# Performance work log

Measured on AMD Instinct MI355X. Metric: run time of the kernel, lower is better.

The kernel has to match this reference:

```python
import jax, jax.numpy as jnp
import numpy as np

N = 50000      # nodes
E = 100000     # edges
F_NODE = 128
F_EDGE = 16
H = 64         # hidden_dim
OUT = 32
STEPS = 3
G = 64         # num_graphs (static; batch.max()+1 in torch)


def setup_inputs() -> dict:
    key = jax.random.key(0)
    ks = jax.random.split(key, 20)

    def lin(k, fin, fout):
        s = 1.0 / np.sqrt(fin)
        return jax.random.uniform(k, (fin, fout), jnp.float32, -s, s)

    def bias(k, fin, fout):
        s = 1.0 / np.sqrt(fin)
        return jax.random.uniform(k, (fout,), jnp.float32, -s, s)

    inp = {
        'x': jax.random.normal(ks[0], (N, F_NODE), jnp.float32),
        'edge_index': jax.random.randint(ks[1], (2, E), 0, N),
        'edge_attr': jax.random.normal(ks[2], (E, F_EDGE), jnp.float32),
        'batch': jnp.sort(jax.random.randint(ks[3], (N,), 0, G)),
        # node encoder
        'W_enc': lin(ks[4], F_NODE, H), 'b_enc': bias(ks[5], F_NODE, H),
        # edge_nn: Linear(F_EDGE,H) -> ReLU -> Linear(H, H*H)
        'W_e1': lin(ks[6], F_EDGE, H), 'b_e1': bias(ks[7], F_EDGE, H),
        'W_e2': lin(ks[8], H, H * H), 'b_e2': bias(ks[9], H, H * H),
        # GRUCell (torch layout: [3H, H])
        'W_ih': jax.random.uniform(ks[10], (3 * H, H), jnp.float32, -1/np.sqrt(H), 1/np.sqrt(H)),
        'W_hh': jax.random.uniform(ks[11], (3 * H, H), jnp.float32, -1/np.sqrt(H), 1/np.sqrt(H)),
        'b_ih': jax.random.uniform(ks[12], (3 * H,), jnp.float32, -1/np.sqrt(H), 1/np.sqrt(H)),
        'b_hh': jax.random.uniform(ks[13], (3 * H,), jnp.float32, -1/np.sqrt(H), 1/np.sqrt(H)),
        # readout MLP: Linear(H,H) -> ReLU -> Linear(H,OUT)
        'W_r1': lin(ks[14], H, H), 'b_r1': bias(ks[15], H, H),
        'W_r2': lin(ks[16], H, OUT), 'b_r2': bias(ks[17], H, OUT),
    }
    return inp


def gru_cell(m, h, W_ih, W_hh, b_ih, b_hh):
    gi = m @ W_ih.T + b_ih   # [N, 3H]
    gh = h @ W_hh.T + b_hh
    i_r, i_z, i_n = jnp.split(gi, 3, axis=-1)
    h_r, h_z, h_n = jnp.split(gh, 3, axis=-1)
    r = jax.nn.sigmoid(i_r + h_r)
    z = jax.nn.sigmoid(i_z + h_z)
    n = jnp.tanh(i_n + r * h_n)
    return (1.0 - z) * n + z * h


def reference(x, edge_index, edge_attr, batch, W_enc, b_enc, W_e1, b_e1,
              W_e2, b_e2, W_ih, W_hh, b_ih, b_hh, W_r1, b_r1, W_r2, b_r2):
    h = x @ W_enc + b_enc                                   # [N, H]
    src, dst = edge_index[0], edge_index[1]
    # edge-conditioned weight matrices (loop-invariant; compute once)
    ew = (jax.nn.relu(edge_attr @ W_e1 + b_e1) @ W_e2 + b_e2).reshape(E, H, H)
    for _ in range(STEPS):
        msg = jnp.einsum('eij,ej->ei', ew, h[src])          # per-edge matvec
        m_agg = jax.ops.segment_sum(msg, dst, num_segments=N)
        h = gru_cell(m_agg, h, W_ih, W_hh, b_ih, b_hh)
    g = jax.ops.segment_sum(h, batch, num_segments=G)       # sum readout
    return jax.nn.relu(g @ W_r1 + b_r1) @ W_r2 + b_r2
```

## Files before the change

kernel.cpp:

```cpp
#include <hip/hip_runtime.h>
#include <hip/hip_fp16.h>
#include <math.h>

#define NN 50000
#define NE 100000
#define FN 128
#define FE 16
#define HD 64
#define OUTD 32
#define NG 64
#define ZK 65
#define EB 256
#define NBMSG ((NE + EB - 1) / EB)

typedef unsigned int uint;
typedef unsigned short ushort;
typedef __attribute__((ext_vector_type(8))) short short8;
typedef __attribute__((ext_vector_type(8))) _Float16 half8;
typedef __attribute__((ext_vector_type(2))) _Float16 half2v;
typedef __attribute__((ext_vector_type(16))) float f32x16;

static __device__ __forceinline__ ushort f2h(float f) {
    _Float16 h = (_Float16)f;
    return __builtin_bit_cast(ushort, h);
}
static __device__ __forceinline__ float h2f(ushort u) {
    return (float)__builtin_bit_cast(_Float16, u);
}
static __device__ __forceinline__ uint pkh2(float a, float b) {
    auto r = __builtin_amdgcn_cvt_pkrtz(a, b);
    return __builtin_bit_cast(uint, r);
}
static __device__ __forceinline__ uint hmul2u(uint a, uint b) {
    half2v x = __builtin_bit_cast(half2v, a);
    half2v y = __builtin_bit_cast(half2v, b);
    half2v r = x * y;
    return __builtin_bit_cast(uint, r);
}
static __device__ __forceinline__ half8 u4h8(uint4 u) {
    return __builtin_bit_cast(half8, u);
}
static __device__ __forceinline__ float fsigmoid(float x) {
    return 1.f / (1.f + __expf(-x));
}
static __device__ __forceinline__ float ftanh(float x) {
    float t = __expf(2.f * x);
    return 1.f - 2.f / (t + 1.f);
}

#define PREP_S0 (ZK * 4096)
#define PREP_S1 (256 * 128)
#define PREP_S2 (64 * 128)
__global__ void k_prep(const float* __restrict__ W_e2, const float* __restrict__ b_e2,
                       const float* __restrict__ W_ih, const float* __restrict__ W_hh,
                       const float* __restrict__ W_enc,
                       ushort* __restrict__ Wtb, ushort* __restrict__ Bg,
                       ushort* __restrict__ Wet) {
    int idx = blockIdx.x * 256 + threadIdx.x;
    if (idx < PREP_S0) {
        int k0 = idx >> 12, r = idx & 4095;
        int jb = r >> 9, rem = r & 511;
        int i = rem >> 3, hh = rem & 7;
        int j = jb * 8 + hh;
        float v = (k0 < 64) ? W_e2[k0 * 4096 + i * 64 + j] : b_e2[i * 64 + j];
        Wtb[idx] = f2h(v);
        return;
    }
    idx -= PREP_S0;
    if (idx < PREP_S1) {
        int n = idx >> 7, k = idx & 127;
        int g = n >> 6, i = n & 63;
        float v = 0.f;
        if (g == 0)      v = (k < 64) ? W_ih[i * 64 + k]         : W_hh[i * 64 + (k - 64)];
        else if (g == 1) v = (k < 64) ? W_ih[(64 + i) * 64 + k]  : W_hh[(64 + i) * 64 + (k - 64)];
        else if (g == 2) v = (k < 64) ? W_ih[(128 + i) * 64 + k] : 0.f;
        else             v = (k < 64) ? 0.f                      : W_hh[(128 + i) * 64 + (k - 64)];
        Bg[idx] = f2h(v);
        return;
    }
    idx -= PREP_S1;
    if (idx < PREP_S2) {
        int n = idx >> 7, k = idx & 127;
        Wet[idx] = f2h(W_enc[k * 64 + n]);
    }
}

#define NBENC ((NN + 127) / 128)
#define NBEDG ((NE + 255) / 256)
__global__ __launch_bounds__(256, 2)
void k_enc_edge(const float* __restrict__ x, const ushort* __restrict__ Wet,
                const float* __restrict__ b_enc,
                const float* __restrict__ ea, const float* __restrict__ W_e1,
                const float* __restrict__ b_e1,
                ushort* __restrict__ hb,
                ushort* __restrict__ zbT, float* __restrict__ magg) {
    int t = threadIdx.x;
    if (blockIdx.x < NBENC) {
        __shared__ __align__(16) ushort blds[64 * 128];
        int wave = t >> 6, lane = t & 63, l31 = lane & 31, lhi = lane >> 5;
        #pragma unroll
        for (int call = 0; call < 4; call++) {
            int slot = call * 256 + t;
            int n = slot >> 4, p = slot & 15;
            int ssrc = p ^ (n & 15);
            const ushort* src = Wet + n * 128 + ssrc * 8;
            __builtin_amdgcn_global_load_lds(
                (const __attribute__((address_space(1))) void*)src,
                (__attribute__((address_space(3))) void*)&blds[(size_t)slot * 8],
                16, 0, 0);
        }
        int node0 = blockIdx.x * 128 + wave * 32;
        int m = node0 + l31;
        int mc = (m < NN) ? m : NN - 1;
        uint4 afr[8];
        const float* xr = x + (size_t)mc * 128;
        #pragma unroll
        for (int ks = 0; ks < 8; ks++) {
            float4 v0 = *(const float4*)(xr + ks * 16 + lhi * 8);
            float4 v1 = *(const float4*)(xr + ks * 16 + lhi * 8 + 4);
            uint4 u;
            u.x = pkh2(v0.x, v0.y); u.y = pkh2(v0.z, v0.w);
            u.z = pkh2(v1.x, v1.y); u.w = pkh2(v1.z, v1.w);
            afr[ks] = u;
        }
        __syncthreads();
        #pragma unroll
        for (int ct = 0; ct < 2; ct++) {
            f32x16 acc = {0};
            int n = ct * 32 + l31;
            #pragma unroll
            for (int ks = 0; ks < 8; ks++) {
                int sp = (ks * 2 + lhi) ^ (n & 15);
                short8 bf = *(const short8*)&blds[n * 128 + sp * 8];
                acc = __builtin_amdgcn_mfma_f32_32x32x16_f16(
                    u4h8(afr[ks]), __builtin_bit_cast(half8, bf), acc, 0, 0, 0);
            }
            int o = ct * 32 + l31;
            float bias = b_enc[o];
            #pragma unroll
            for (int r = 0; r < 16; r++) {
                int row = (r & 3) + 8 * (r >> 2) + 4 * lhi;
                int node = node0 + row;
                if (node < NN) {
                    float v = acc[r] + bias;
                    hb[node * 64 + o] = f2h(v);
                    magg[node * 64 + o] = 0.f;
                }
            }
        }
    } else {
        __shared__ float Ws[16 * 64];
        __shared__ float b1s[64];
        for (int idx = t; idx < 1024; idx += 256) Ws[idx] = W_e1[idx];
        if (t < 64) b1s[t] = b_e1[t];
        __syncthreads();
        int e = (blockIdx.x - NBENC) * 256 + t;
        int ec = (e < NE) ? e : NE - 1;
        float eav[16];
        const float4* ep = (const float4*)(ea + ec * 16);
        #pragma unroll
        for (int q = 0; q < 4; q++) {
            float4 v = ep[q];
            eav[q * 4 + 0] = v.x; eav[q * 4 + 1] = v.y; eav[q * 4 + 2] = v.z; eav[q * 4 + 3] = v.w;
        }
        if (e >= NE) return;
        #pragma unroll 4
        for (int k = 0; k < 64; k++) {
            float acc = b1s[k];
            #pragma unroll
            for (int f = 0; f < 16; f++) acc += eav[f] * Ws[f * 64 + k];
            zbT[(size_t)k * NE + e] = f2h(fmaxf(acc, 0.f));
        }
    }
}

__global__ __launch_bounds__(256, 2)
void k_message(const ushort* __restrict__ zbT, const ushort* __restrict__ hb,
               const int* __restrict__ eidx, const ushort* __restrict__ Wtb,
               float* __restrict__ m_agg) {
    __shared__ __align__(16) ushort wlds[2][2 * 4096];
    __shared__ __align__(16) ushort zlds[64 * 256];
    __shared__ int sdst[256];

    int t = threadIdx.x;
    int wave = t >> 6, lane = t & 63;
    int l31 = lane & 31, lhi = lane >> 5;
    int eblk = blockIdx.x * EB;
    int e0 = eblk + wave * 64;

    {
        int e = eblk + t; if (e >= NE) e = NE - 1;
        sdst[t] = eidx[NE + e];
    }

    uint hw[2][16];
    #pragma unroll
    for (int mt = 0; mt < 2; mt++) {
        int e = e0 + mt * 32 + l31;
        int ec = (e < NE) ? e : NE - 1;
        int s = eidx[ec];
        const ushort* hrow = hb + (size_t)s * 64;
        #pragma unroll
        for (int c = 0; c < 4; c++) {
            uint4 v = *(const uint4*)(hrow + c * 16 + lhi * 8);
            hw[mt][c * 4 + 0] = v.x; hw[mt][c * 4 + 1] = v.y;
            hw[mt][c * 4 + 2] = v.z; hw[mt][c * 4 + 3] = v.w;
        }
    }

    #pragma unroll
    for (int call = 0; call < 8; call++) {
        int slot = call * 256 + t;
        int k0 = slot >> 5, p = slot & 31;
        const ushort* src = zbT + (size_t)k0 * NE + eblk + p * 8;
        __builtin_amdgcn_global_load_lds(
            (const __attribute__((address_space(1))) void*)src,
            (__attribute__((address_space(3))) void*)&zlds[(size_t)slot * 8],
            16, 0, 0);
    }

    auto stagew = [&](int slab0, int buf) {
        #pragma unroll
        for (int call = 0; call < 4; call++) {
            int slot = call * 256 + t;
            int slab = slab0 + (slot >> 9);
            if (slab > 64) slab = 64;
            int wofs = slot & 511;
            const ushort* src = Wtb + (size_t)slab * 4096 + wofs * 8;
            __builtin_amdgcn_global_load_lds(
                (const __attribute__((address_space(1))) void*)src,
                (__attribute__((address_space(3))) void*)&wlds[buf][(size_t)slot * 8],
                16, 0, 0);
        }
    };
    stagew(0, 0);

    f32x16 acc00 = {0}, acc01 = {0}, acc10 = {0}, acc11 = {0};

    for (int rnd = 0; rnd < 33; rnd++) {
        __syncthreads();
        int buf = rnd & 1;
        if (rnd < 32) stagew(2 * rnd + 2, buf ^ 1);
        int nk = (rnd < 32) ? 2 : 1;
        for (int kk = 0; kk < nk; kk++) {
            int k0 = 2 * rnd + kk;
            uint zz0, zz1;
            if (k0 < 64) {
                uint za = zlds[k0 * 256 + wave * 64 + l31];
                uint zb = zlds[k0 * 256 + wave * 64 + 32 + l31];
                zz0 = za | (za << 16);
                zz1 = zb | (zb << 16);
            } else {
                zz0 = 0x3C003C00u; zz1 = 0x3C003C00u;
            }
            const ushort* wb = &wlds[buf][kk * 4096];
            #pragma unroll
            for (int c = 0; c < 4; c++) {
                int jb = c * 2 + lhi;
                short8 b0r = *(const short8*)&wb[jb * 512 + l31 * 8];
                short8 b1r = *(const short8*)&wb[jb * 512 + 256 + l31 * 8];
                uint4 au0, au1;
                au0.x = hmul2u(zz0, hw[0][c * 4 + 0]); au0.y = hmul2u(zz0, hw[0][c * 4 + 1]);
                au0.z = hmul2u(zz0, hw[0][c * 4 + 2]); au0.w = hmul2u(zz0, hw[0][c * 4 + 3]);
                au1.x = hmul2u(zz1, hw[1][c * 4 + 0]); au1.y = hmul2u(zz1, hw[1][c * 4 + 1]);
                au1.z = hmul2u(zz1, hw[1][c * 4 + 2]); au1.w = hmul2u(zz1, hw[1][c * 4 + 3]);
                half8 a0 = u4h8(au0), a1 = u4h8(au1);
                half8 b0 = __builtin_bit_cast(half8, b0r);
                half8 b1 = __builtin_bit_cast(half8, b1r);
                acc00 = __builtin_amdgcn_mfma_f32_32x32x16_f16(a0, b0, acc00, 0, 0, 0);
                acc01 = __builtin_amdgcn_mfma_f32_32x32x16_f16(a0, b1, acc01, 0, 0, 0);
                acc10 = __builtin_amdgcn_mfma_f32_32x32x16_f16(a1, b0, acc10, 0, 0, 0);
                acc11 = __builtin_amdgcn_mfma_f32_32x32x16_f16(a1, b1, acc11, 0, 0, 0);
            }
        }
    }

    #pragma unroll
    for (int r = 0; r < 16; r++) {
        int roff = (r & 3) + 8 * (r >> 2) + 4 * lhi;
        int eA = e0 + roff, eB = e0 + 32 + roff;
        if (eA < NE) {
            int d0 = sdst[wave * 64 + roff];
            atomicAdd(m_agg + (size_t)d0 * 64 + l31,      acc00[r]);
            atomicAdd(m_agg + (size_t)d0 * 64 + 32 + l31, acc01[r]);
        }
        if (eB < NE) {
            int d1 = sdst[wave * 64 + 32 + roff];
            atomicAdd(m_agg + (size_t)d1 * 64 + l31,      acc10[r]);
            atomicAdd(m_agg + (size_t)d1 * 64 + 32 + l31, acc11[r]);
        }
    }
}

__global__ __launch_bounds__(256, 2)
void k_gru(float* __restrict__ magg,
           const ushort* __restrict__ hb, const ushort* __restrict__ Bg,
           const float* __restrict__ b_ih, const float* __restrict__ b_hh,
           ushort* __restrict__ hb_out, int zero_m) {
    __shared__ __align__(16) ushort blds[256 * 128];
    int t = threadIdx.x;
    int wave = t >> 6, lane = t & 63, l31 = lane & 31, lhi = lane >> 5;
    #pragma unroll
    for (int call = 0; call < 16; call++) {
        int slot = call * 256 + t;
        int n = slot >> 4, p = slot & 15;
        int ssrc = p ^ (n & 15);
        const ushort* src = Bg + n * 128 + ssrc * 8;
        __builtin_amdgcn_global_load_lds(
            (const __attribute__((address_space(1))) void*)src,
            (__attribute__((address_space(3))) void*)&blds[(size_t)slot * 8],
            16, 0, 0);
    }
    int node0 = blockIdx.x * 128 + wave * 32;
    int m = node0 + l31;
    int mc = (m < NN) ? m : NN - 1;
    uint4 afr[8];
    const float* mrow = magg + (size_t)mc * 64;
    #pragma unroll
    for (int ks = 0; ks < 4; ks++) {
        float4 v0 = *(const float4*)(mrow + ks * 16 + lhi * 8);
        float4 v1 = *(const float4*)(mrow + ks * 16 + lhi * 8 + 4);
        uint4 u;
        u.x = pkh2(v0.x, v0.y); u.y = pkh2(v0.z, v0.w);
        u.z = pkh2(v1.x, v1.y); u.w = pkh2(v1.z, v1.w);
        afr[ks] = u;
    }
    const ushort* hrow = hb + (size_t)mc * 64;
    #pragma unroll
    for (int ks = 4; ks < 8; ks++) {
        afr[ks] = *(const uint4*)(hrow + (ks - 4) * 16 + lhi * 8);
    }
    __syncthreads();
    if (zero_m) {
        float4 zz = {0.f, 0.f, 0.f, 0.f};
        float* mw = magg + (size_t)mc * 64;
        #pragma unroll
        for (int ks = 0; ks < 4; ks++) {
            *(float4*)(mw + ks * 16 + lhi * 8) = zz;
            *(float4*)(mw + ks * 16 + lhi * 8 + 4) = zz;
        }
    }
    #pragma unroll
    for (int ct = 0; ct < 2; ct++) {
        f32x16 aR = {0}, aZ = {0}, aI = {0}, aH = {0};
        int nR = 0   + ct * 32 + l31;
        int nZ = 64  + ct * 32 + l31;
        int nI = 128 + ct * 32 + l31;
        int nH = 192 + ct * 32 + l31;
        #pragma unroll
        for (int ks = 0; ks < 8; ks++) {
            int s = ks * 2 + lhi;
            half8 a = u4h8(afr[ks]);
            short8 bR = *(const short8*)&blds[nR * 128 + (s ^ (nR & 15)) * 8];
            short8 bZ = *(const short8*)&blds[nZ * 128 + (s ^ (nZ & 15)) * 8];
            short8 bI = *(const short8*)&blds[nI * 128 + (s ^ (nI & 15)) * 8];
            short8 bH = *(const short8*)&blds[nH * 128 + (s ^ (nH & 15)) * 8];
            aR = __builtin_amdgcn_mfma_f32_32x32x16_f16(a, __builtin_bit_cast(half8, bR), aR, 0, 0, 0);
            aZ = __builtin_amdgcn_mfma_f32_32x32x16_f16(a, __builtin_bit_cast(half8, bZ), aZ, 0, 0, 0);
            aI = __builtin_amdgcn_mfma_f32_32x32x16_f16(a, __builtin_bit_cast(half8, bI), aI, 0, 0, 0);
            aH = __builtin_amdgcn_mfma_f32_32x32x16_f16(a, __builtin_bit_cast(half8, bH), aH, 0, 0, 0);
        }
        int i = ct * 32 + l31;
        float brv = b_ih[i] + b_hh[i];
        float bzv = b_ih[64 + i] + b_hh[64 + i];
        float biv = b_ih[128 + i];
        float bhv = b_hh[128 + i];
        #pragma unroll
        for (int r = 0; r < 16; r++) {
            int row = (r & 3) + 8 * (r >> 2) + 4 * lhi;
            int node = node0 + row;
            if (node < NN) {
                float ho = h2f(hb[node * 64 + i]);
                float rg = fsigmoid(aR[r] + brv);
                float zg = fsigmoid(aZ[r] + bzv);
                float ng = ftanh(aI[r] + biv + rg * (aH[r] + bhv));
                float hv = (1.f - zg) * ng + zg * ho;
                hb_out[node * 64 + i] = f2h(hv);
            }
        }
    }
}

__global__ __launch_bounds__(256)
void k_scatter_g(const ushort* __restrict__ hb, const int* __restrict__ batch,
                 float* __restrict__ g) {
    int t = threadIdx.x;
    int i = t & 63, sub = t >> 6;
    int n0 = blockIdx.x * 64 + sub * 16;
    if (n0 >= NN) return;
    float acc = 0.f;
    int curg = batch[n0];
    for (int q = 0; q < 16; q++) {
        int n = n0 + q;
        if (n >= NN) break;
        int gq = batch[n];
        if (gq != curg) {
            atomicAdd(&g[curg * 64 + i], acc);
            acc = 0.f; curg = gq;
        }
        acc += h2f(hb[n * 64 + i]);
    }
    atomicAdd(&g[curg * 64 + i], acc);
}

__global__ __launch_bounds__(1024)
void k_readout(const float* __restrict__ g, const float* __restrict__ W1, const float* __restrict__ b1,
               const float* __restrict__ W2, const float* __restrict__ b2, float* __restrict__ out) {
    __shared__ float gs[64 * 64];
    __shared__ float ts[64 * 64];
    int t = threadIdx.x;
    for (int idx = t; idx < 4096; idx += 1024) gs[idx] = g[idx];
    __syncthreads();
    for (int idx = t; idx < 4096; idx += 1024) {
        int r = idx >> 6, c = idx & 63;
        float acc = b1[c];
        #pragma unroll 8
        for (int k = 0; k < 64; k++) acc += gs[r * 64 + k] * W1[k * 64 + c];
        ts[idx] = fmaxf(acc, 0.f);
    }
    __syncthreads();
    for (int idx = t; idx < 2048; idx += 1024) {
        int r = idx >> 5, c = idx & 31;
        float acc = b2[c];
        #pragma unroll 8
        for (int k = 0; k < 64; k++) acc += ts[r * 64 + k] * W2[k * 32 + c];
        out[idx] = acc;
    }
}

extern "C" void kernel_launch(void* const* d_in, const int* in_sizes, int n_in,
                              void* d_out, int out_size, void* d_ws, size_t ws_size,
                              hipStream_t stream) {
    const float* x     = (const float*)d_in[0];
    const int*   ei    = (const int*)  d_in[1];
    const float* ea    = (const float*)d_in[2];
    const int*   batch = (const int*)  d_in[3];
    const float* W_enc = (const float*)d_in[4];
    const float* b_enc = (const float*)d_in[5];
    const float* W_e1  = (const float*)d_in[6];
    const float* b_e1  = (const float*)d_in[7];
    const float* W_e2  = (const float*)d_in[8];
    const float* b_e2  = (const float*)d_in[9];
    const float* W_ih  = (const float*)d_in[10];
    const float* W_hh  = (const float*)d_in[11];
    const float* b_ih  = (const float*)d_in[12];
    const float* b_hh  = (const float*)d_in[13];
    const float* W_r1  = (const float*)d_in[14];
    const float* b_r1  = (const float*)d_in[15];
    const float* W_r2  = (const float*)d_in[16];
    const float* b_r2  = (const float*)d_in[17];
    float* out = (float*)d_out;

    float* ws    = (float*)d_ws;
    float* magg  = ws;
    float* g     = magg + NN * 64;
    ushort* hb   = (ushort*)(g + NG * 64);
    ushort* hb2  = hb   + NN * 64;
    ushort* zbT  = hb2  + NN * 64;
    ushort* Wtb  = zbT  + (size_t)ZK * NE;
    ushort* Bgru = Wtb  + ZK * 4096;
    ushort* Wet  = Bgru + 256 * 128;

    hipLaunchKernelGGL(k_prep, dim3((PREP_S0 + PREP_S1 + PREP_S2 + 255) / 256), dim3(256), 0, stream,
                       W_e2, b_e2, W_ih, W_hh, W_enc, Wtb, Bgru, Wet);
    hipLaunchKernelGGL(k_enc_edge, dim3(NBENC + NBEDG), dim3(256), 0, stream,
                       x, Wet, b_enc, ea, W_e1, b_e1, hb, zbT, magg);

    ushort* hbc = hb; ushort* hbn = hb2;
    for (int s = 0; s < 3; s++) {
        hipLaunchKernelGGL(k_message, dim3(NBMSG), dim3(256), 0, stream,
                           zbT, hbc, ei, Wtb, magg);
        hipLaunchKernelGGL(k_gru,     dim3((NN + 127) / 128), dim3(256), 0, stream,
                           magg, hbc, Bgru, b_ih, b_hh, hbn, (s < 2) ? 1 : 0);
        ushort* tb = hbc; hbc = hbn; hbn = tb;
    }

    hipMemsetAsync(g, 0, (size_t)NG * 64 * sizeof(float), stream);
    hipLaunchKernelGGL(k_scatter_g, dim3((NN + 63) / 64), dim3(256), 0, stream, hbc, batch, g);
    hipLaunchKernelGGL(k_readout,   dim3(1), dim3(1024), 0, stream, g, W_r1, b_r1, W_r2, b_r2, out);
}
```

Baseline: 396.8 us.

## Drop LDS staging in message and GRU kernels to raise occupancy

The message kernel no longer stages the per-edge z coefficients for the whole block in a 32KB LDS buffer. Each wave now reads them straight from global memory with a one-round register prefetch, which shrinks LDS use and raises the occupancy hint from 2 to 4. The GRU kernel drops its 64KB LDS copy of the gate weights. Its weights are pre-permuted in the prep kernel into MFMA fragment order so each lane reads them directly from global memory, and work is split so two waves share 32 nodes by output half. This trades LDS staging for more global loads, which may or may not be served by cache, and adds small scattered z loads inside the message loop.

After: 463.4 us. 1.17x slower.

```diff
diff --git a/kernel.cpp b/kernel.cpp
--- a/kernel.cpp
+++ b/kernel.cpp
@@ -68,8 +68,14 @@
     }
     idx -= PREP_S0;
     if (idx < PREP_S1) {
-        int n = idx >> 7, k = idx & 127;
-        int g = n >> 6, i = n & 63;
+        int hh = idx & 7;
+        int l31 = (idx >> 3) & 31;
+        int lhi = (idx >> 8) & 1;
+        int ks  = (idx >> 9) & 7;
+        int ihr = (idx >> 12) & 1;
+        int g   = (idx >> 13) & 3;
+        int i = ihr * 32 + l31;
+        int k = ks * 16 + lhi * 8 + hh;
         float v = 0.f;
         if (g == 0)      v = (k < 64) ? W_ih[i * 64 + k]         : W_hh[i * 64 + (k - 64)];
         else if (g == 1) v = (k < 64) ? W_ih[(64 + i) * 64 + k]  : W_hh[(64 + i) * 64 + (k - 64)];
@@ -174,12 +180,11 @@
     }
 }
 
-__global__ __launch_bounds__(256, 2)
+__global__ __launch_bounds__(256, 4)
 void k_message(const ushort* __restrict__ zbT, const ushort* __restrict__ hb,
                const int* __restrict__ eidx, const ushort* __restrict__ Wtb,
                float* __restrict__ m_agg) {
     __shared__ __align__(16) ushort wlds[2][2 * 4096];
-    __shared__ __align__(16) ushort zlds[64 * 256];
     __shared__ int sdst[256];
 
     int t = threadIdx.x;
@@ -208,16 +213,9 @@
         }
     }
 
-    #pragma unroll
-    for (int call = 0; call < 8; call++) {
-        int slot = call * 256 + t;
-        int k0 = slot >> 5, p = slot & 31;
-        const ushort* src = zbT + (size_t)k0 * NE + eblk + p * 8;
-        __builtin_amdgcn_global_load_lds(
-            (const __attribute__((address_space(1))) void*)src,
-            (__attribute__((address_space(3))) void*)&zlds[(size_t)slot * 8],
-            16, 0, 0);
-    }
+    const ushort* zb0 = zbT + e0;
+    uint zc0 = zb0[l31],      zc1 = zb0[32 + l31];
+    uint zc2 = zb0[NE + l31], zc3 = zb0[NE + 32 + l31];
 
     auto stagew = [&](int slab0, int buf) {
         #pragma unroll
@@ -241,13 +239,20 @@
         __syncthreads();
         int buf = rnd & 1;
         if (rnd < 32) stagew(2 * rnd + 2, buf ^ 1);
+        uint zn0 = 0, zn1 = 0, zn2 = 0, zn3 = 0;
+        if (rnd < 31) {
+            const ushort* zr2 = zbT + (size_t)(2 * rnd + 2) * NE + e0;
+            const ushort* zr3 = zbT + (size_t)(2 * rnd + 3) * NE + e0;
+            zn0 = zr2[l31]; zn1 = zr2[32 + l31];
+            zn2 = zr3[l31]; zn3 = zr3[32 + l31];
+        }
         int nk = (rnd < 32) ? 2 : 1;
         for (int kk = 0; kk < nk; kk++) {
             int k0 = 2 * rnd + kk;
             uint zz0, zz1;
             if (k0 < 64) {
-                uint za = zlds[k0 * 256 + wave * 64 + l31];
-                uint zb = zlds[k0 * 256 + wave * 64 + 32 + l31];
+                uint za = kk ? zc2 : zc0;
+                uint zb = kk ? zc3 : zc1;
                 zz0 = za | (za << 16);
                 zz1 = zb | (zb << 16);
             } else {
@@ -273,6 +278,7 @@
                 acc11 = __builtin_amdgcn_mfma_f32_32x32x16_f16(a1, b1, acc11, 0, 0, 0);
             }
         }
+        zc0 = zn0; zc1 = zn1; zc2 = zn2; zc3 = zn3;
     }
 
     #pragma unroll
@@ -292,26 +298,16 @@
     }
 }
 
-__global__ __launch_bounds__(256, 2)
+#define NBGRU ((NN + 63) / 64)
+__global__ __launch_bounds__(256, 3)
 void k_gru(float* __restrict__ magg,
-           const ushort* __restrict__ hb, const ushort* __restrict__ Bg,
+           const ushort* __restrict__ hb, const ushort* __restrict__ Bg2,
            const float* __restrict__ b_ih, const float* __restrict__ b_hh,
            ushort* __restrict__ hb_out, int zero_m) {
-    __shared__ __align__(16) ushort blds[256 * 128];
     int t = threadIdx.x;
-    int wave = t >> 6, lane = t & 63, l31 = lane & 31, lhi = lane >> 5;
-    #pragma unroll
-    for (int call = 0; call < 16; call++) {
-        int slot = call * 256 + t;
-        int n = slot >> 4, p = slot & 15;
-        int ssrc = p ^ (n & 15);
-        const ushort* src = Bg + n * 128 + ssrc * 8;
-        __builtin_amdgcn_global_load_lds(
-            (const __attribute__((address_space(1))) void*)src,
-            (__attribute__((address_space(3))) void*)&blds[(size_t)slot * 8],
-            16, 0, 0);
-    }
-    int node0 = blockIdx.x * 128 + wave * 32;
+    int w = t >> 6, lane = t & 63, l31 = lane & 31, lhi = lane >> 5;
+    int nh = w >> 1, ih = w & 1;
+    int node0 = blockIdx.x * 64 + nh * 32;
     int m = node0 + l31;
     int mc = (m < NN) ? m : NN - 1;
     uint4 afr[8];
@@ -331,7 +327,7 @@
         afr[ks] = *(const uint4*)(hrow + (ks - 4) * 16 + lhi * 8);
     }
     __syncthreads();
-    if (zero_m) {
+    if (zero_m && ih == 0) {
         float4 zz = {0.f, 0.f, 0.f, 0.f};
         float* mw = magg + (size_t)mc * 64;
         #pragma unroll
@@ -340,43 +336,36 @@
             *(float4*)(mw + ks * 16 + lhi * 8 + 4) = zz;
         }
     }
-    #pragma unroll
-    for (int ct = 0; ct < 2; ct++) {
-        f32x16 aR = {0}, aZ = {0}, aI = {0}, aH = {0};
-        int nR = 0   + ct * 32 + l31;
-        int nZ = 64  + ct * 32 + l31;
-        int nI = 128 + ct * 32 + l31;
-        int nH = 192 + ct * 32 + l31;
-        #pragma unroll
-        for (int ks = 0; ks < 8; ks++) {
-            int s = ks * 2 + lhi;
-            half8 a = u4h8(afr[ks]);
-            short8 bR = *(const short8*)&blds[nR * 128 + (s ^ (nR & 15)) * 8];
-            short8 bZ = *(const short8*)&blds[nZ * 128 + (s ^ (nZ & 15)) * 8];
-            short8 bI = *(const short8*)&blds[nI * 128 + (s ^ (nI & 15)) * 8];
-            short8 bH = *(const short8*)&blds[nH * 128 + (s ^ (nH & 15)) * 8];
-            aR = __builtin_amdgcn_mfma_f32_32x32x16_f16(a, __builtin_bit_cast(half8, bR), aR, 0, 0, 0);
-            aZ = __builtin_amdgcn_mfma_f32_32x32x16_f16(a, __builtin_bit_cast(half8, bZ), aZ, 0, 0, 0);
-            aI = __builtin_amdgcn_mfma_f32_32x32x16_f16(a, __builtin_bit_cast(half8, bI), aI, 0, 0, 0);
-            aH = __builtin_amdgcn_mfma_f32_32x32x16_f16(a, __builtin_bit_cast(half8, bH), aH, 0, 0, 0);
-        }
-        int i = ct * 32 + l31;
-        float brv = b_ih[i] + b_hh[i];
-        float bzv = b_ih[64 + i] + b_hh[64 + i];
-        float biv = b_ih[128 + i];
-        float bhv = b_hh[128 + i];
-        #pragma unroll
-        for (int r = 0; r < 16; r++) {
-            int row = (r & 3) + 8 * (r >> 2) + 4 * lhi;
-            int node = node0 + row;
-            if (node < NN) {
-                float ho = h2f(hb[node * 64 + i]);
-                float rg = fsigmoid(aR[r] + brv);
-                float zg = fsigmoid(aZ[r] + bzv);
-                float ng = ftanh(aI[r] + biv + rg * (aH[r] + bhv));
-                float hv = (1.f - zg) * ng + zg * ho;
-                hb_out[node * 64 + i] = f2h(hv);
-            }
+    f32x16 aR = {0}, aZ = {0}, aI = {0}, aH = {0};
+    #pragma unroll
+    for (int ks = 0; ks < 8; ks++) {
+        half8 a = u4h8(afr[ks]);
+        size_t ofs = (size_t)((ih * 8 + ks) * 2 + lhi) * 256 + l31 * 8;
+        short8 bR = *(const short8*)&Bg2[ofs];
+        short8 bZ = *(const short8*)&Bg2[ofs + 32 * 256];
+        short8 bI = *(const short8*)&Bg2[ofs + 64 * 256];
+        short8 bH = *(const short8*)&Bg2[ofs + 96 * 256];
+        aR = __builtin_amdgcn_mfma_f32_32x32x16_f16(a, __builtin_bit_cast(half8, bR), aR, 0, 0, 0);
+        aZ = __builtin_amdgcn_mfma_f32_32x32x16_f16(a, __builtin_bit_cast(half8, bZ), aZ, 0, 0, 0);
+        aI = __builtin_amdgcn_mfma_f32_32x32x16_f16(a, __builtin_bit_cast(half8, bI), aI, 0, 0, 0);
+        aH = __builtin_amdgcn_mfma_f32_32x32x16_f16(a, __builtin_bit_cast(half8, bH), aH, 0, 0, 0);
+    }
+    int i = ih * 32 + l31;
+    float brv = b_ih[i] + b_hh[i];
+    float bzv = b_ih[64 + i] + b_hh[64 + i];
+    float biv = b_ih[128 + i];
+    float bhv = b_hh[128 + i];
+    #pragma unroll
+    for (int r = 0; r < 16; r++) {
+        int row = (r & 3) + 8 * (r >> 2) + 4 * lhi;
+        int node = node0 + row;
+        if (node < NN) {
+            float ho = h2f(hb[node * 64 + i]);
+            float rg = fsigmoid(aR[r] + brv);
+            float zg = fsigmoid(aZ[r] + bzv);
+            float ng = ftanh(aI[r] + biv + rg * (aH[r] + bhv));
+            float hv = (1.f - zg) * ng + zg * ho;
+            hb_out[node * 64 + i] = f2h(hv);
         }
     }
 }
@@ -470,7 +459,7 @@
     for (int s = 0; s < 3; s++) {
         hipLaunchKernelGGL(k_message, dim3(NBMSG), dim3(256), 0, stream,
                            zbT, hbc, ei, Wtb, magg);
-        hipLaunchKernelGGL(k_gru,     dim3((NN + 127) / 128), dim3(256), 0, stream,
+        hipLaunchKernelGGL(k_gru,     dim3(NBGRU), dim3(256), 0, stream,
                            magg, hbc, Bgru, b_ih, b_hh, hbn, (s < 2) ? 1 : 0);
         ushort* tb = hbc; hbc = hbn; hbn = tb;
     }
```
